# Optimization experiments

Hardware: AMD Instinct MI355X
Metric: run time of the kernel (lower is better)

## Reference

```python
import jax, jax.numpy as jnp
import numpy as np

N, E, G = 50000, 400000, 64   # nodes, edges, graphs
HEADS = 4
F_IN, H1, C3, OUT = 64, 96, 64, 10  # in feats, hidden (3*32), last conv out, classes


def seg_softmax(alpha, index, num_segments):
    # numerically stable softmax over segments (PyG softmax(alpha, edge_index_i))
    amax = jax.ops.segment_max(alpha, index, num_segments)
    amax = jnp.where(jnp.isfinite(amax), amax, 0.0)
    e = jnp.exp(alpha - amax[index])
    denom = jax.ops.segment_sum(e, index, num_segments)
    return e / (denom[index] + 1e-16)


def general_conv(x, src, dst, Wm, bm, att, Ws=None, bs=None):
    # GeneralConv (attention=True, additive, directed_msg, aggr='add')
    C = att.shape[-1]
    m = (x[src] @ Wm + bm).reshape(-1, HEADS, C)              # [E,H,C] gathered messages
    a = jax.nn.leaky_relu((m * att).sum(-1), 0.2)             # [E,H] attention logits
    a = seg_softmax(a, dst, N)                                # segment softmax per dest node
    agg = jax.ops.segment_sum(m * a[..., None], dst, N)       # [N,H,C] scatter-add
    out = agg.mean(axis=1)                                    # head mean -> [N,C]
    if Ws is None:                                            # lin_self = Identity (in==out)
        return out + x
    return out + x @ Ws + bs


def setup_inputs():
    key = jax.random.key(0)
    ks = jax.random.split(key, 16)
    s = 0.05
    return {
        "x": jax.random.normal(ks[0], (N, F_IN), jnp.float32),
        "edge_index": jax.random.randint(ks[1], (2, E), 0, N, jnp.int32),
        "batch": jnp.sort(jax.random.randint(ks[2], (N,), 0, G, jnp.int32)),
        # layer 1: F_IN -> H1
        "Wm1": jax.random.normal(ks[3], (F_IN, HEADS * H1), jnp.float32) * s,
        "bm1": jnp.zeros((HEADS * H1,), jnp.float32),
        "att1": jax.random.normal(ks[4], (HEADS, H1), jnp.float32) * s,
        "Ws1": jax.random.normal(ks[5], (F_IN, H1), jnp.float32) * s,
        "bs1": jnp.zeros((H1,), jnp.float32),
        # layer 2: H1 -> H1 (lin_self = Identity)
        "Wm2": jax.random.normal(ks[6], (H1, HEADS * H1), jnp.float32) * s,
        "bm2": jnp.zeros((HEADS * H1,), jnp.float32),
        "att2": jax.random.normal(ks[7], (HEADS, H1), jnp.float32) * s,
        # layer 3: H1 -> C3
        "Wm3": jax.random.normal(ks[8], (H1, HEADS * C3), jnp.float32) * s,
        "bm3": jnp.zeros((HEADS * C3,), jnp.float32),
        "att3": jax.random.normal(ks[9], (HEADS, C3), jnp.float32) * s,
        "Ws3": jax.random.normal(ks[10], (H1, C3), jnp.float32) * s,
        "bs3": jnp.zeros((C3,), jnp.float32),
        # classifier
        "Wfc": jax.random.normal(ks[11], (C3, OUT), jnp.float32) * s,
        "bfc": jnp.zeros((OUT,), jnp.float32),
    }


def reference(x, edge_index, batch, Wm1, bm1, att1, Ws1, bs1,
              Wm2, bm2, att2, Wm3, bm3, att3, Ws3, bs3, Wfc, bfc):
    src, dst = edge_index[0], edge_index[1]
    h = general_conv(x, src, dst, Wm1, bm1, att1, Ws1, bs1)
    h = general_conv(h, src, dst, Wm2, bm2, att2)
    h = general_conv(h, src, dst, Wm3, bm3, att3, Ws3, bs3)
    # global_mean_pool
    ssum = jax.ops.segment_sum(h, batch, G)
    cnt = jax.ops.segment_sum(jnp.ones((N, 1), h.dtype), batch, G)
    pooled = ssum / jnp.maximum(cnt, 1.0)                      # [G,C3]
    logits = pooled @ Wfc + bfc
    return jax.nn.log_softmax(logits, axis=1)
```

## Files before the change

kernel.cpp:

```cpp
#include <hip/hip_runtime.h>
#include <hip/hip_bf16.h>
#include <stdint.h>

using bf16 = __hip_bfloat16;
typedef __attribute__((ext_vector_type(8))) short bf16x8;
typedef __attribute__((ext_vector_type(4))) float f32x4;
typedef __attribute__((ext_vector_type(2))) float f32x2;

#define NN 50000
#define NE 400000
#define NG 64
#define FIN 64
#define HID 96
#define CC3 64
#define NOUT 10

#define SCAN_BLOCK 256
#define NPART ((NN + SCAN_BLOCK - 1) / SCAN_BLOCK)

__device__ __forceinline__ float b2f(bf16 h){ return __bfloat162float(h); }
__device__ __forceinline__ bf16 f2b(float f){ return __float2bfloat16(f); }
__device__ __forceinline__ float blo(unsigned v){ return __uint_as_float(v << 16); }
__device__ __forceinline__ float bhi(unsigned v){ return __uint_as_float(v & 0xFFFF0000u); }

struct PrepA {
  const float *Wm1,*att1,*bm1,*Wm2,*att2,*bm2,*Wm3,*att3,*bm3,*bs1;
  float *f2,*f3,*lbv,*zb; bf16* WTf1;
  int* deg; float* psum; int* done;
};
__global__ __launch_bounds__(256) void prep_a_kernel(PrepA j){
  int bid = blockIdx.x;
  if (bid == 0){
    for (int i=threadIdx.x; i<96*4; i+=256){
      int k=i>>2, h=i&3; float a=0.f;
      for (int c=0;c<96;++c) a += j.Wm2[k*384 + h*96 + c]*j.att2[h*96+c];
      j.f2[i]=a;
    }
    for (int i=threadIdx.x; i<96*4; i+=256){
      int k=i>>2, h=i&3; float a=0.f;
      for (int c=0;c<64;++c) a += j.Wm3[k*256 + h*64 + c]*j.att3[h*64+c];
      j.f3[i]=a;
    }
    for (int i=threadIdx.x; i<16*64; i+=256){
      int col=i>>6, k=i&63; float a=0.f;
      if (col<4){ for (int c=0;c<96;++c) a += j.Wm1[k*384 + col*96 + c]*j.att1[col*96+c]; }
      j.WTf1[i] = f2b(a);
    }
    if (threadIdx.x < 96) j.zb[threadIdx.x] = 0.f;
    __syncthreads();
    if (threadIdx.x < 4){
      int h = threadIdx.x;
      float l1=0.f,l2=0.f,l3=0.f;
      for (int c=0;c<96;++c) l1 += j.bm1[h*96+c]*j.att1[h*96+c];
      for (int c=0;c<96;++c) l2 += j.bm2[h*96+c]*j.att2[h*96+c];
      for (int c=0;c<64;++c) l3 += j.bm3[h*64+c]*j.att3[h*64+c];
      float e2 = l2;
      for (int k=0;k<96;++k) e2 += j.bs1[k]*j.f2[k*4+h];
      j.lbv[h]=l1; j.lbv[4+h]=e2; j.lbv[8+h]=l3;
    }
  } else if (bid <= NPART){
    int i=(bid-1)*256+threadIdx.x;
    if (i<NN) j.deg[i]=0;
  } else {
    for (int i=threadIdx.x; i<NG*CC3; i+=256) j.psum[i]=0.f;
    if (threadIdx.x==0) *j.done = 0;
  }
}

struct PrepB {
  const float *Wm1,*bm1,*Ws1,*Wm2,*bm2,*Wm3,*bm3,*Ws3;
  const float *f2,*f3;
  bf16 *WT1,*WT2,*WT3;
};
__device__ __forceinline__ float w1full(const PrepB& j, int k, int c){
  if (k < 256) return 0.25f*j.Wm1[(k&63)*384 + (k>>6)*96 + c];
  if (k == 256) return 0.25f*(j.bm1[c]+j.bm1[96+c]+j.bm1[192+c]+j.bm1[288+c]);
  if (k < 288) return 0.f;
  return j.Ws1[(k-288)*96 + c];
}
__device__ __forceinline__ float w2full(const PrepB& j, int k, int c){
  if (k < 384){ int kk=k%96, h=k/96; return 0.25f*j.Wm2[kk*384 + h*96 + c]; }
  if (k == 384) return 0.25f*(j.bm2[c]+j.bm2[96+c]+j.bm2[192+c]+j.bm2[288+c]);
  if (k < 416) return 0.f;
  return (k-416==c) ? 1.f : 0.f;
}
__device__ __forceinline__ float w3full(const PrepB& j, int k, int c){
  if (k < 384){ int kk=k%96, h=k/96; return 0.25f*j.Wm3[kk*256 + h*64 + c]; }
  if (k == 384) return 0.25f*(j.bm3[c]+j.bm3[64+c]+j.bm3[128+c]+j.bm3[192+c]);
  if (k < 416) return 0.f;
  return j.Ws3[(k-416)*64 + c];
}
__global__ __launch_bounds__(256) void prep_b_kernel(PrepB j){
  int idx = blockIdx.x*256 + threadIdx.x;
  if (idx < 112*384){
    int col = idx/384, k = idx - col*384;
    float v;
    if (k >= 352) v = 0.f;
    else if (col < 96) v = w1full(j,k,col);
    else if (col < 100){ int h=col-96; float a=0.f;
      for (int c=0;c<96;++c) a += w1full(j,k,c)*j.f2[c*4+h]; v=a; }
    else v = 0.f;
    j.WT1[col*384 + k] = f2b(v);
  } else if (idx < 112*384 + 112*512){
    int r = idx - 112*384;
    int col = r/512, k = r - col*512;
    float v;
    if (col < 96) v = w2full(j,k,col);
    else if (col < 100){ int h=col-96; float a=0.f;
      for (int c=0;c<96;++c) a += w2full(j,k,c)*j.f3[c*4+h]; v=a; }
    else v = 0.f;
    j.WT2[col*512 + k] = f2b(v);
  } else {
    int r = idx - 112*384 - 112*512;
    int col = r/512, k = r - col*512;
    j.WT3[col*512 + k] = f2b(w3full(j,k,col));
  }
}

__global__ void deg_kernel(const int* __restrict__ ei, int* __restrict__ deg){
  int e = blockIdx.x*256 + threadIdx.x;
  if (e < NE) atomicAdd(&deg[ei[NE + e]], 1);
}

__global__ __launch_bounds__(256) void scan_part_kernel(const int* __restrict__ deg,
    int* __restrict__ partials, int* __restrict__ done, int* __restrict__ off){
  __shared__ int ws[4];
  __shared__ int lastflag;
  __shared__ int buf[256];
  int i = blockIdx.x*SCAN_BLOCK + threadIdx.x;
  int v = (i < NN) ? deg[i] : 0;
  int lane = threadIdx.x & 63, w = threadIdx.x >> 6;
  int s = v;
  #pragma unroll
  for (int m=1;m<64;m<<=1) s += __shfl_xor(s,m);
  if (lane==0) ws[w]=s;
  __syncthreads();
  if (threadIdx.x==0){
    int tot = ws[0]+ws[1]+ws[2]+ws[3];
    atomicExch(&partials[blockIdx.x], tot);
    __threadfence();
    int old = atomicAdd(done, 1);
    lastflag = (old == NPART-1) ? 1 : 0;
  }
  __syncthreads();
  if (lastflag){
    int t = threadIdx.x;
    int pv = (t < NPART) ? atomicAdd(&partials[t], 0) : 0;
    buf[t] = pv; __syncthreads();
    for (int st=1; st<256; st<<=1){
      int x = (t>=st) ? buf[t-st] : 0;
      __syncthreads();
      buf[t] += x;
      __syncthreads();
    }
    if (t < NPART) atomicExch(&partials[t], buf[t] - pv);
    if (t == 0) off[NN] = buf[255];
  }
}

__global__ __launch_bounds__(256) void scan_final_kernel(const int* __restrict__ deg,
    const int* __restrict__ partials, int* __restrict__ off, int* __restrict__ cursor){
  __shared__ int buf[256];
  int i = blockIdx.x*SCAN_BLOCK + threadIdx.x;
  int t = threadIdx.x;
  int v = (i<NN) ? deg[i] : 0;
  buf[t] = v; __syncthreads();
  for (int s=1;s<256;s<<=1){
    int x = (t>=s) ? buf[t-s] : 0;
    __syncthreads();
    buf[t] += x;
    __syncthreads();
  }
  int ex = partials[blockIdx.x] + buf[t] - v;
  if (i<NN){ off[i]=ex; cursor[i]=ex; }
}

__global__ void scatter_kernel(const int* __restrict__ ei, int* __restrict__ cursor,
                               int* __restrict__ csr_src){
  int e = blockIdx.x*256 + threadIdx.x;
  if (e < NE){
    int d = ei[NE + e];
    int slot = atomicAdd(&cursor[d], 1);
    csr_src[slot] = ei[e];
  }
}

__global__ __launch_bounds__(256) void el1_kernel(const float* __restrict__ x,
    const bf16* __restrict__ WTf1, const float* __restrict__ lbv,
    bf16* __restrict__ xb, uint8_t* __restrict__ x8, float* __restrict__ EL)
{
  const int wave = threadIdx.x>>6, lane = threadIdx.x&63;
  const int tile = blockIdx.x*4 + wave;
  if (tile >= NN/16) return;
  const int lm = lane&15, q = lane>>4;
  const size_t row = (size_t)tile*16 + lm;
  bf16x8 xf[2];
  #pragma unroll
  for (int kt=0;kt<2;++kt){
    float4 a0 = *(const float4*)(x + row*64 + kt*32 + q*8);
    float4 a1 = *(const float4*)(x + row*64 + kt*32 + q*8 + 4);
    bf16 t[8] = {f2b(a0.x),f2b(a0.y),f2b(a0.z),f2b(a0.w),
                 f2b(a1.x),f2b(a1.y),f2b(a1.z),f2b(a1.w)};
    xf[kt] = *(const bf16x8*)t;
    *(bf16x8*)(xb + row*64 + kt*32 + q*8) = xf[kt];
    int p0 = 0, p1 = 0;
    p0 = __builtin_amdgcn_cvt_pk_fp8_f32(a0.x, a0.y, p0, false);
    p0 = __builtin_amdgcn_cvt_pk_fp8_f32(a0.z, a0.w, p0, true);
    p1 = __builtin_amdgcn_cvt_pk_fp8_f32(a1.x, a1.y, p1, false);
    p1 = __builtin_amdgcn_cvt_pk_fp8_f32(a1.z, a1.w, p1, true);
    uint2 pk; pk.x = (unsigned)p0; pk.y = (unsigned)p1;
    *(uint2*)(x8 + row*64 + kt*32 + q*8) = pk;
  }
  f32x4 acc = {};
  #pragma unroll
  for (int kt=0;kt<2;++kt){
    bf16x8 wf = *(const bf16x8*)(WTf1 + (size_t)lm*64 + kt*32 + q*8);
    acc = __builtin_amdgcn_mfma_f32_16x16x32_bf16(wf, xf[kt], acc, 0,0,0);
  }
  if (q==0){
    float4 e; float l;
    l=acc[0]+lbv[0]; l=(l>=0.f)?l:0.2f*l; e.x=__expf(fminf(fmaxf(l,-60.f),60.f));
    l=acc[1]+lbv[1]; l=(l>=0.f)?l:0.2f*l; e.y=__expf(fminf(fmaxf(l,-60.f),60.f));
    l=acc[2]+lbv[2]; l=(l>=0.f)?l:0.2f*l; e.z=__expf(fminf(fmaxf(l,-60.f),60.f));
    l=acc[3]+lbv[3]; l=(l>=0.f)?l:0.2f*l; e.w=__expf(fminf(fmaxf(l,-60.f),60.f));
    *(float4*)(EL + 4*row) = e;
  }
}

template<int KH>
__global__ __launch_bounds__(256) void agg_kernel(
    const int* __restrict__ off, const int* __restrict__ csr_src,
    const float* __restrict__ ELin, const uint8_t* __restrict__ T8,
    bf16* __restrict__ Sb)
{
  constexpr int R  = 4*KH;
  constexpr int KS = R + 32;
  const int wave = threadIdx.x >> 6, lane = threadIdx.x & 63;
  const int n = blockIdx.x*4 + wave;
  const int e0 = off[n], e1 = off[n+1];

  if (KH == 64){
    const int hidx = lane >> 4;
    const int kk = (4*lane) & 63;
    float acc[4] = {0.f,0.f,0.f,0.f};
    float dnl = 0.f;
    int base = e0;
    int cnt  = min(8, e1-base);
    int sreg = (base < e1 && lane < cnt) ? csr_src[base+lane] : 0;
    while (base < e1){
      const int nbase = base + 8;
      const int ncnt  = min(8, e1-nbase);
      int nreg = (nbase < e1 && lane < ncnt) ? csr_src[nbase+lane] : 0;
      int sv[8];
      #pragma unroll
      for (int j=0;j<8;++j) sv[j] = __shfl(sreg, j);
      float wl[8]; unsigned u[8];
      #pragma unroll
      for (int j=0;j<8;++j){
        wl[j] = ELin[4*(size_t)sv[j] + hidx];
        u[j]  = *(const unsigned*)(T8 + (size_t)sv[j]*64 + kk);
      }
      #pragma unroll
      for (int j=0;j<8;++j){
        float w = (j < cnt) ? wl[j] : 0.f;
        dnl += w;
        f32x2 a0 = __builtin_amdgcn_cvt_pk_f32_fp8((int)u[j], false);
        f32x2 a1 = __builtin_amdgcn_cvt_pk_f32_fp8((int)u[j], true);
        acc[0] += a0.x*w;  acc[1] += a0.y*w;
        acc[2] += a1.x*w;  acc[3] += a1.y*w;
      }
      sreg = nreg; cnt = ncnt; base = nbase;
    }
    const float rd = 1.f/(dnl + 1e-16f);
    bf16* srow = Sb + (size_t)n*KS;
    bf16 st[4] = {f2b(acc[0]*rd), f2b(acc[1]*rd), f2b(acc[2]*rd), f2b(acc[3]*rd)};
    *(uint2*)(srow + hidx*64 + kk) = *(const uint2*)st;
    if (lane < 8){
      uint2 z; z.x = 0u; z.y = 0u;
      if (lane == 0 && e1 > e0) z.x = 0x3F80u;
      *(uint2*)(srow + R + lane*4) = z;
    }
  } else {
    const bool act = (8*lane) < R;
    const int hidx = min(3, (8*lane)/KH);
    const int kk = (8*lane) % KH;
    float acc[8] = {0.f,0.f,0.f,0.f,0.f,0.f,0.f,0.f};
    float dnl = 0.f;
    int base = e0;
    int cnt  = min(8, e1-base);
    int sreg = (base < e1 && lane < cnt) ? csr_src[base+lane] : 0;
    while (base < e1){
      const int nbase = base + 8;
      const int ncnt  = min(8, e1-nbase);
      int nreg = (nbase < e1 && lane < ncnt) ? csr_src[nbase+lane] : 0;
      int sv[8];
      #pragma unroll
      for (int j=0;j<8;++j) sv[j] = __shfl(sreg, j);
      float wl[8]; uint2 u[8];
      #pragma unroll
      for (int j=0;j<8;++j){
        wl[j] = ELin[4*(size_t)sv[j] + hidx];
        u[j]  = *(const uint2*)(T8 + (size_t)sv[j]*KH + kk);
      }
      #pragma unroll
      for (int j=0;j<8;++j){
        float w = (j < cnt) ? wl[j] : 0.f;
        dnl += w;
        f32x2 a0 = __builtin_amdgcn_cvt_pk_f32_fp8((int)u[j].x, false);
        f32x2 a1 = __builtin_amdgcn_cvt_pk_f32_fp8((int)u[j].x, true);
        f32x2 a2 = __builtin_amdgcn_cvt_pk_f32_fp8((int)u[j].y, false);
        f32x2 a3 = __builtin_amdgcn_cvt_pk_f32_fp8((int)u[j].y, true);
        acc[0] += a0.x*w;  acc[1] += a0.y*w;
        acc[2] += a1.x*w;  acc[3] += a1.y*w;
        acc[4] += a2.x*w;  acc[5] += a2.y*w;
        acc[6] += a3.x*w;  acc[7] += a3.y*w;
      }
      sreg = nreg; cnt = ncnt; base = nbase;
    }
    const float rd = 1.f/(dnl + 1e-16f);
    bf16* srow = Sb + (size_t)n*KS;
    if (act){
      bf16 st[8];
      #pragma unroll
      for (int t=0;t<8;++t) st[t] = f2b(acc[t]*rd);
      *(bf16x8*)(srow + 8*lane) = *(const bf16x8*)st;
    } else if (8*lane < KS){
      bf16 st[8] = {};
      if (8*lane == R) st[0] = f2b((e1 > e0) ? 1.f : 0.f);
      *(bf16x8*)(srow + 8*lane) = *(const bf16x8*)st;
    }
  }
}

template<int KH, int NCT, bool POOL>
__global__ __launch_bounds__(256, 4) void gemm_kernel(
    const bf16* __restrict__ Sb, const bf16* __restrict__ Hprev,
    const bf16* __restrict__ WT, const float* __restrict__ bias,
    const float* __restrict__ lbe, bf16* __restrict__ Hout,
    uint8_t* __restrict__ H8out, float* __restrict__ ELout,
    const int* __restrict__ batch, float* __restrict__ psum)
{
  constexpr int R      = 4*KH;
  constexpr int KS     = R + 32;
  constexpr int KA     = KS + KH;
  constexpr int KTS    = KS/32;
  constexpr int NKT    = KA/32;
  constexpr int NCHUNK = (NKT + 3)/4;
  constexpr int KAP    = NCHUNK*128;
  constexpr int NCOL   = NCT*16;
  constexpr int NT     = NN/16;
  constexpr int WSZ    = NCOL*256;
  constexpr int OSZ    = POOL ? (4*16*68*4) : (4*16*104*2);
  constexpr int USZ    = (WSZ > OSZ) ? WSZ : OSZ;
  __shared__ __align__(16) unsigned char lds[USZ];

  const int tid  = threadIdx.x;
  const int wave = tid >> 6, lane = tid & 63;
  const int lm = lane & 15, q = lane >> 4;
  const int tile = blockIdx.x*4 + wave;
  const bool active = (tile < NT);
  const size_t row = (size_t)tile*16 + lm;

  const bf16* arow = Sb + row*KS;
  const bf16* hrow = Hprev + row*KH;
  const unsigned sw = (unsigned)((lm & 7) << 4);

  f32x4 acc[NCT];
  #pragma unroll
  for (int c=0;c<NCT;++c) acc[c] = (f32x4){0.f,0.f,0.f,0.f};

  #pragma unroll
  for (int chunk=0; chunk<NCHUNK; ++chunk){
    if (chunk) __syncthreads();
    {
      const int k0 = chunk*128;
      for (int idx = tid; idx < NCOL*16; idx += 256){
        const int col = idx >> 4, sg = idx & 15;
        uint4 v = *(const uint4*)(WT + (size_t)col*KAP + k0 + sg*8);
        const unsigned off = (unsigned)(sg*16) ^ (unsigned)((col & 7) << 4);
        *(uint4*)(lds + col*256 + off) = v;
      }
    }
    __syncthreads();
    if (active){
      bf16x8 a[4];
      #pragma unroll
      for (int t=0;t<4;++t){
        const int kt = chunk*4 + t;
        if (kt < KTS)      a[t] = *(const bf16x8*)(arow + kt*32 + q*8);
        else if (kt < NKT) a[t] = *(const bf16x8*)(hrow + (kt-KTS)*32 + q*8);
        else { bf16 z[8] = {}; a[t] = *(const bf16x8*)z; }
      }
      #pragma unroll
      for (int ct=0; ct<NCT; ++ct){
        const unsigned char* rbase = lds + (ct*16 + lm)*256;
        #pragma unroll
        for (int t=0;t<4;++t){
          bf16x8 wf = *(const bf16x8*)(rbase + (((unsigned)(t*64 + q*16)) ^ sw));
          acc[ct] = __builtin_amdgcn_mfma_f32_16x16x32_bf16(wf, a[t], acc[ct], 0,0,0);
        }
      }
    }
  }
  __syncthreads();

  if (active){
    if (!POOL){
      unsigned short* ob = (unsigned short*)(lds) + wave*16*104;
      #pragma unroll
      for (int ct=0; ct<NCT-1; ++ct){
        const int c = ct*16 + q*4;
        bf16 st[4] = {f2b(acc[ct][0]+bias[c]),   f2b(acc[ct][1]+bias[c+1]),
                      f2b(acc[ct][2]+bias[c+2]), f2b(acc[ct][3]+bias[c+3])};
        *(uint2*)(ob + lm*104 + c) = *(const uint2*)st;
      }
      if (q == 0){
        float4 e; float l;
        l=acc[NCT-1][0]+lbe[0]; l=(l>=0.f)?l:0.2f*l; e.x=__expf(fminf(fmaxf(l,-60.f),60.f));
        l=acc[NCT-1][1]+lbe[1]; l=(l>=0.f)?l:0.2f*l; e.y=__expf(fminf(fmaxf(l,-60.f),60.f));
        l=acc[NCT-1][2]+lbe[2]; l=(l>=0.f)?l:0.2f*l; e.z=__expf(fminf(fmaxf(l,-60.f),60.f));
        l=acc[NCT-1][3]+lbe[3]; l=(l>=0.f)?l:0.2f*l; e.w=__expf(fminf(fmaxf(l,-60.f),60.f));
        *(float4*)(ELout + 4*row) = e;
      }
      __builtin_amdgcn_wave_barrier();
      const size_t n0w = (size_t)tile*16;
      #pragma unroll
      for (int jj=0; jj<3; ++jj){
        const int idx = jj*64 + lane;
        const int r = idx/12, ch = idx - r*12;
        uint4 v = *(const uint4*)(ob + r*104 + ch*8);
        *(uint4*)(Hout + (n0w+r)*96 + ch*8) = v;
        int p0 = 0, p1 = 0;
        p0 = __builtin_amdgcn_cvt_pk_fp8_f32(blo(v.x), bhi(v.x), p0, false);
        p0 = __builtin_amdgcn_cvt_pk_fp8_f32(blo(v.y), bhi(v.y), p0, true);
        p1 = __builtin_amdgcn_cvt_pk_fp8_f32(blo(v.z), bhi(v.z), p1, false);
        p1 = __builtin_amdgcn_cvt_pk_fp8_f32(blo(v.w), bhi(v.w), p1, true);
        uint2 pk; pk.x = (unsigned)p0; pk.y = (unsigned)p1;
        *(uint2*)(H8out + (n0w+r)*96 + ch*8) = pk;
      }
    } else {
      float* ob = (float*)(lds) + wave*16*68;
      #pragma unroll
      for (int ct=0; ct<NCT; ++ct){
        const int c = ct*16 + q*4;
        float* orow = ob + lm*68;
        orow[c]   = acc[ct][0]+bias[c];   orow[c+1] = acc[ct][1]+bias[c+1];
        orow[c+2] = acc[ct][2]+bias[c+2]; orow[c+3] = acc[ct][3]+bias[c+3];
      }
      int bload = (lane < 16) ? batch[tile*16 + lane] : 0;
      __builtin_amdgcn_wave_barrier();
      const int c = lane;
      int curg = __shfl(bload, 0); float a = 0.f;
      #pragma unroll
      for (int i=0;i<16;++i){
        float v = ob[i*68 + c];
        int g = __shfl(bload, i);
        if (g != curg){ atomicAdd(&psum[curg*64+c], a); a=0.f; curg=g; }
        a += v;
      }
      atomicAdd(&psum[curg*64+c], a);
    }
  }
}

__global__ __launch_bounds__(64) void fc_kernel(const float* __restrict__ psum,
    const int* __restrict__ batch, const float* __restrict__ Wfc,
    const float* __restrict__ bfc, float* __restrict__ out){
  int g = blockIdx.x, t = threadIdx.x;
  __shared__ int sb[2];
  if (t < 2){
    int target = g + t;
    int lo=0, hi=NN;
    while (lo<hi){ int mid=(lo+hi)>>1; if (batch[mid]<target) lo=mid+1; else hi=mid; }
    sb[t]=lo;
  }
  __syncthreads();
  float cnt = (float)(sb[1]-sb[0]);
  __shared__ float p[CC3];
  __shared__ float lg[NOUT];
  p[t] = psum[g*CC3 + t] / fmaxf(cnt, 1.0f);
  __syncthreads();
  if (t < NOUT){
    float a = bfc[t];
    for (int c=0;c<CC3;++c) a += p[c]*Wfc[c*NOUT + t];
    lg[t] = a;
  }
  __syncthreads();
  if (t < NOUT){
    float m = -INFINITY;
    #pragma unroll
    for (int i=0;i<NOUT;++i) m = fmaxf(m, lg[i]);
    float s = 0.f;
    #pragma unroll
    for (int i=0;i<NOUT;++i) s += __expf(lg[i]-m);
    out[g*NOUT + t] = lg[t] - m - __logf(s);
  }
}

extern "C" void kernel_launch(void* const* d_in, const int* in_sizes, int n_in,
                              void* d_out, int out_size, void* d_ws, size_t ws_size,
                              hipStream_t stream) {
  const float* xf    = (const float*)d_in[0];
  const int*   ei    = (const int*)d_in[1];
  const int*   batch = (const int*)d_in[2];
  const float* pWm1  = (const float*)d_in[3];
  const float* pbm1  = (const float*)d_in[4];
  const float* patt1 = (const float*)d_in[5];
  const float* pWs1  = (const float*)d_in[6];
  const float* pbs1  = (const float*)d_in[7];
  const float* pWm2  = (const float*)d_in[8];
  const float* pbm2  = (const float*)d_in[9];
  const float* patt2 = (const float*)d_in[10];
  const float* pWm3  = (const float*)d_in[11];
  const float* pbm3  = (const float*)d_in[12];
  const float* patt3 = (const float*)d_in[13];
  const float* pWs3  = (const float*)d_in[14];
  const float* pbs3  = (const float*)d_in[15];
  const float* pWfc  = (const float*)d_in[16];
  const float* pbfc  = (const float*)d_in[17];

  char* p = (char*)d_ws;
  auto alloc = [&](size_t bytes)->char*{ char* q = p; p += (bytes + 255) & ~(size_t)255; return q; };
  int*     deg     = (int*)  alloc(NN*sizeof(int));
  int*     off     = (int*)  alloc((NN+1)*sizeof(int));
  int*     cursor  = (int*)  alloc(NN*sizeof(int));
  int*     csr_src = (int*)  alloc(NE*sizeof(int));
  int*     partials= (int*)  alloc(NPART*sizeof(int));
  int*     done    = (int*)  alloc(sizeof(int));
  float*   ELa     = (float*)alloc((size_t)NN*4*sizeof(float));
  float*   ELb     = (float*)alloc((size_t)NN*4*sizeof(float));
  bf16*    xb      = (bf16*) alloc((size_t)NN*64*sizeof(bf16));
  uint8_t* x8      = (uint8_t*)alloc((size_t)NN*64);
  uint8_t* H8      = (uint8_t*)alloc((size_t)NN*96);
  bf16*    H1b     = (bf16*) alloc((size_t)NN*96*sizeof(bf16));
  bf16*    H2b     = (bf16*) alloc((size_t)NN*96*sizeof(bf16));
  bf16*    Sb      = (bf16*) alloc((size_t)NN*416*sizeof(bf16));
  float*   psum    = (float*)alloc((size_t)NG*CC3*sizeof(float));
  float*   f2      = (float*)alloc(96*4*sizeof(float));
  float*   f3      = (float*)alloc(96*4*sizeof(float));
  float*   lbv     = (float*)alloc(12*sizeof(float));
  float*   zb      = (float*)alloc(96*sizeof(float));
  bf16*    WTf1    = (bf16*) alloc((size_t)16*64*sizeof(bf16));
  bf16*    WT1     = (bf16*) alloc((size_t)112*384*sizeof(bf16));
  bf16*    WT2     = (bf16*) alloc((size_t)112*512*sizeof(bf16));
  bf16*    WT3     = (bf16*) alloc((size_t)64*512*sizeof(bf16));

  PrepA pa;
  pa.Wm1=pWm1; pa.att1=patt1; pa.bm1=pbm1;
  pa.Wm2=pWm2; pa.att2=patt2; pa.bm2=pbm2;
  pa.Wm3=pWm3; pa.att3=patt3; pa.bm3=pbm3;
  pa.bs1=pbs1; pa.f2=f2; pa.f3=f3; pa.lbv=lbv; pa.zb=zb; pa.WTf1=WTf1;
  pa.deg=deg; pa.psum=psum; pa.done=done;
  prep_a_kernel<<<NPART+2, 256, 0, stream>>>(pa);

  PrepB pb;
  pb.Wm1=pWm1; pb.bm1=pbm1; pb.Ws1=pWs1;
  pb.Wm2=pWm2; pb.bm2=pbm2;
  pb.Wm3=pWm3; pb.bm3=pbm3; pb.Ws3=pWs3;
  pb.f2=f2; pb.f3=f3; pb.WT1=WT1; pb.WT2=WT2; pb.WT3=WT3;
  prep_b_kernel<<<(112*384 + 112*512 + 64*512)/256, 256, 0, stream>>>(pb);

  deg_kernel<<<(NE+255)/256, 256, 0, stream>>>(ei, deg);
  scan_part_kernel<<<NPART, 256, 0, stream>>>(deg, partials, done, off);
  scan_final_kernel<<<NPART, 256, 0, stream>>>(deg, partials, off, cursor);
  scatter_kernel<<<(NE+255)/256, 256, 0, stream>>>(ei, cursor, csr_src);

  el1_kernel<<<(NN/16+3)/4, 256, 0, stream>>>(xf, WTf1, lbv, xb, x8, ELa);

  const int AGB = NN/4;
  const int GGB = (NN/16 + 3)/4;

  agg_kernel<64><<<AGB, 256, 0, stream>>>(off, csr_src, ELa, x8, Sb);
  gemm_kernel<64,7,false><<<GGB, 256, 0, stream>>>(Sb, xb, WT1, pbs1, lbv+4,
                                                   H1b, H8, ELb, batch, psum);
  agg_kernel<96><<<AGB, 256, 0, stream>>>(off, csr_src, ELb, H8, Sb);
  gemm_kernel<96,7,false><<<GGB, 256, 0, stream>>>(Sb, H1b, WT2, zb, lbv+8,
                                                   H2b, H8, ELa, batch, psum);
  agg_kernel<96><<<AGB, 256, 0, stream>>>(off, csr_src, ELa, H8, Sb);
  gemm_kernel<96,4,true ><<<GGB, 256, 0, stream>>>(Sb, H2b, WT3, pbs3, nullptr,
                                                   nullptr, nullptr, nullptr, batch, psum);

  fc_kernel<<<NG, 64, 0, stream>>>(psum, batch, pWfc, pbfc, (float*)d_out);
}
```

Measured before the change: 337.1 us.

## Fuse el1 into prep_b launch and hoist gemm A-operand loads out of chunk loop

```diff
diff --git a/kernel.cpp b/kernel.cpp
--- a/kernel.cpp
+++ b/kernel.cpp
@@ -17,6 +17,8 @@
 
 #define SCAN_BLOCK 256
 #define NPART ((NN + SCAN_BLOCK - 1) / SCAN_BLOCK)
+#define PBW ((112*384 + 112*512 + 64*512)/256)
+#define ELB ((NN/16 + 3)/4)
 
 __device__ __forceinline__ float b2f(bf16 h){ return __bfloat162float(h); }
 __device__ __forceinline__ bf16 f2b(float f){ return __float2bfloat16(f); }
@@ -71,6 +73,8 @@
   const float *Wm1,*bm1,*Ws1,*Wm2,*bm2,*Wm3,*bm3,*Ws3;
   const float *f2,*f3;
   bf16 *WT1,*WT2,*WT3;
+  const float* x; const bf16* WTf1; const float* lbv;
+  bf16* xb; uint8_t* x8; float* EL;
 };
 __device__ __forceinline__ float w1full(const PrepB& j, int k, int c){
   if (k < 256) return 0.25f*j.Wm1[(k&63)*384 + (k>>6)*96 + c];
@@ -91,29 +95,69 @@
   return j.Ws3[(k-416)*64 + c];
 }
 __global__ __launch_bounds__(256) void prep_b_kernel(PrepB j){
-  int idx = blockIdx.x*256 + threadIdx.x;
-  if (idx < 112*384){
-    int col = idx/384, k = idx - col*384;
-    float v;
-    if (k >= 352) v = 0.f;
-    else if (col < 96) v = w1full(j,k,col);
-    else if (col < 100){ int h=col-96; float a=0.f;
-      for (int c=0;c<96;++c) a += w1full(j,k,c)*j.f2[c*4+h]; v=a; }
-    else v = 0.f;
-    j.WT1[col*384 + k] = f2b(v);
-  } else if (idx < 112*384 + 112*512){
-    int r = idx - 112*384;
-    int col = r/512, k = r - col*512;
-    float v;
-    if (col < 96) v = w2full(j,k,col);
-    else if (col < 100){ int h=col-96; float a=0.f;
-      for (int c=0;c<96;++c) a += w2full(j,k,c)*j.f3[c*4+h]; v=a; }
-    else v = 0.f;
-    j.WT2[col*512 + k] = f2b(v);
+  const int bid = blockIdx.x;
+  if (bid < PBW){
+    int idx = bid*256 + threadIdx.x;
+    if (idx < 112*384){
+      int col = idx/384, k = idx - col*384;
+      float v;
+      if (k >= 352) v = 0.f;
+      else if (col < 96) v = w1full(j,k,col);
+      else if (col < 100){ int h=col-96; float a=0.f;
+        for (int c=0;c<96;++c) a += w1full(j,k,c)*j.f2[c*4+h]; v=a; }
+      else v = 0.f;
+      j.WT1[col*384 + k] = f2b(v);
+    } else if (idx < 112*384 + 112*512){
+      int r = idx - 112*384;
+      int col = r/512, k = r - col*512;
+      float v;
+      if (col < 96) v = w2full(j,k,col);
+      else if (col < 100){ int h=col-96; float a=0.f;
+        for (int c=0;c<96;++c) a += w2full(j,k,c)*j.f3[c*4+h]; v=a; }
+      else v = 0.f;
+      j.WT2[col*512 + k] = f2b(v);
+    } else {
+      int r = idx - 112*384 - 112*512;
+      int col = r/512, k = r - col*512;
+      j.WT3[col*512 + k] = f2b(w3full(j,k,col));
+    }
   } else {
-    int r = idx - 112*384 - 112*512;
-    int col = r/512, k = r - col*512;
-    j.WT3[col*512 + k] = f2b(w3full(j,k,col));
+    const int wave = threadIdx.x>>6, lane = threadIdx.x&63;
+    const int tile = (bid - PBW)*4 + wave;
+    if (tile >= NN/16) return;
+    const int lm = lane&15, q = lane>>4;
+    const size_t row = (size_t)tile*16 + lm;
+    bf16x8 xf[2];
+    #pragma unroll
+    for (int kt=0;kt<2;++kt){
+      float4 a0 = *(const float4*)(j.x + row*64 + kt*32 + q*8);
+      float4 a1 = *(const float4*)(j.x + row*64 + kt*32 + q*8 + 4);
+      bf16 t[8] = {f2b(a0.x),f2b(a0.y),f2b(a0.z),f2b(a0.w),
+                   f2b(a1.x),f2b(a1.y),f2b(a1.z),f2b(a1.w)};
+      xf[kt] = *(const bf16x8*)t;
+      *(bf16x8*)(j.xb + row*64 + kt*32 + q*8) = xf[kt];
+      int p0 = 0, p1 = 0;
+      p0 = __builtin_amdgcn_cvt_pk_fp8_f32(a0.x, a0.y, p0, false);
+      p0 = __builtin_amdgcn_cvt_pk_fp8_f32(a0.z, a0.w, p0, true);
+      p1 = __builtin_amdgcn_cvt_pk_fp8_f32(a1.x, a1.y, p1, false);
+      p1 = __builtin_amdgcn_cvt_pk_fp8_f32(a1.z, a1.w, p1, true);
+      uint2 pk; pk.x = (unsigned)p0; pk.y = (unsigned)p1;
+      *(uint2*)(j.x8 + row*64 + kt*32 + q*8) = pk;
+    }
+    f32x4 acc = {};
+    #pragma unroll
+    for (int kt=0;kt<2;++kt){
+      bf16x8 wf = *(const bf16x8*)(j.WTf1 + (size_t)lm*64 + kt*32 + q*8);
+      acc = __builtin_amdgcn_mfma_f32_16x16x32_bf16(wf, xf[kt], acc, 0,0,0);
+    }
+    if (q==0){
+      float4 e; float l;
+      l=acc[0]+j.lbv[0]; l=(l>=0.f)?l:0.2f*l; e.x=__expf(fminf(fmaxf(l,-60.f),60.f));
+      l=acc[1]+j.lbv[1]; l=(l>=0.f)?l:0.2f*l; e.y=__expf(fminf(fmaxf(l,-60.f),60.f));
+      l=acc[2]+j.lbv[2]; l=(l>=0.f)?l:0.2f*l; e.z=__expf(fminf(fmaxf(l,-60.f),60.f));
+      l=acc[3]+j.lbv[3]; l=(l>=0.f)?l:0.2f*l; e.w=__expf(fminf(fmaxf(l,-60.f),60.f));
+      *(float4*)(j.EL + 4*row) = e;
+    }
   }
 }
 
@@ -185,48 +229,6 @@
   }
 }
 
-__global__ __launch_bounds__(256) void el1_kernel(const float* __restrict__ x,
-    const bf16* __restrict__ WTf1, const float* __restrict__ lbv,
-    bf16* __restrict__ xb, uint8_t* __restrict__ x8, float* __restrict__ EL)
-{
-  const int wave = threadIdx.x>>6, lane = threadIdx.x&63;
-  const int tile = blockIdx.x*4 + wave;
-  if (tile >= NN/16) return;
-  const int lm = lane&15, q = lane>>4;
-  const size_t row = (size_t)tile*16 + lm;
-  bf16x8 xf[2];
-  #pragma unroll
-  for (int kt=0;kt<2;++kt){
-    float4 a0 = *(const float4*)(x + row*64 + kt*32 + q*8);
-    float4 a1 = *(const float4*)(x + row*64 + kt*32 + q*8 + 4);
-    bf16 t[8] = {f2b(a0.x),f2b(a0.y),f2b(a0.z),f2b(a0.w),
-                 f2b(a1.x),f2b(a1.y),f2b(a1.z),f2b(a1.w)};
-    xf[kt] = *(const bf16x8*)t;
-    *(bf16x8*)(xb + row*64 + kt*32 + q*8) = xf[kt];
-    int p0 = 0, p1 = 0;
-    p0 = __builtin_amdgcn_cvt_pk_fp8_f32(a0.x, a0.y, p0, false);
-    p0 = __builtin_amdgcn_cvt_pk_fp8_f32(a0.z, a0.w, p0, true);
-    p1 = __builtin_amdgcn_cvt_pk_fp8_f32(a1.x, a1.y, p1, false);
-    p1 = __builtin_amdgcn_cvt_pk_fp8_f32(a1.z, a1.w, p1, true);
-    uint2 pk; pk.x = (unsigned)p0; pk.y = (unsigned)p1;
-    *(uint2*)(x8 + row*64 + kt*32 + q*8) = pk;
-  }
-  f32x4 acc = {};
-  #pragma unroll
-  for (int kt=0;kt<2;++kt){
-    bf16x8 wf = *(const bf16x8*)(WTf1 + (size_t)lm*64 + kt*32 + q*8);
-    acc = __builtin_amdgcn_mfma_f32_16x16x32_bf16(wf, xf[kt], acc, 0,0,0);
-  }
-  if (q==0){
-    float4 e; float l;
-    l=acc[0]+lbv[0]; l=(l>=0.f)?l:0.2f*l; e.x=__expf(fminf(fmaxf(l,-60.f),60.f));
-    l=acc[1]+lbv[1]; l=(l>=0.f)?l:0.2f*l; e.y=__expf(fminf(fmaxf(l,-60.f),60.f));
-    l=acc[2]+lbv[2]; l=(l>=0.f)?l:0.2f*l; e.z=__expf(fminf(fmaxf(l,-60.f),60.f));
-    l=acc[3]+lbv[3]; l=(l>=0.f)?l:0.2f*l; e.w=__expf(fminf(fmaxf(l,-60.f),60.f));
-    *(float4*)(EL + 4*row) = e;
-  }
-}
-
 template<int KH>
 __global__ __launch_bounds__(256) void agg_kernel(
     const int* __restrict__ off, const int* __restrict__ csr_src,
@@ -333,7 +335,7 @@
 }
 
 template<int KH, int NCT, bool POOL>
-__global__ __launch_bounds__(256, 4) void gemm_kernel(
+__global__ __launch_bounds__(256, 3) void gemm_kernel(
     const bf16* __restrict__ Sb, const bf16* __restrict__ Hprev,
     const bf16* __restrict__ WT, const float* __restrict__ bias,
     const float* __restrict__ lbe, bf16* __restrict__ Hout,
@@ -359,11 +361,18 @@
   const int lm = lane & 15, q = lane >> 4;
   const int tile = blockIdx.x*4 + wave;
   const bool active = (tile < NT);
-  const size_t row = (size_t)tile*16 + lm;
+  const int ctile = active ? tile : (NT-1);
+  const size_t row = (size_t)ctile*16 + lm;
 
   const bf16* arow = Sb + row*KS;
   const bf16* hrow = Hprev + row*KH;
   const unsigned sw = (unsigned)((lm & 7) << 4);
+
+  bf16x8 a[NKT];
+  #pragma unroll
+  for (int kt=0; kt<KTS; ++kt) a[kt] = *(const bf16x8*)(arow + kt*32 + q*8);
+  #pragma unroll
+  for (int kt=KTS; kt<NKT; ++kt) a[kt] = *(const bf16x8*)(hrow + (kt-KTS)*32 + q*8);
 
   f32x4 acc[NCT];
   #pragma unroll
@@ -374,7 +383,9 @@
     if (chunk) __syncthreads();
     {
       const int k0 = chunk*128;
-      for (int idx = tid; idx < NCOL*16; idx += 256){
+      #pragma unroll
+      for (int it=0; it<NCOL*16/256; ++it){
+        const int idx = it*256 + tid;
         const int col = idx >> 4, sg = idx & 15;
         uint4 v = *(const uint4*)(WT + (size_t)col*KAP + k0 + sg*8);
         const unsigned off = (unsigned)(sg*16) ^ (unsigned)((col & 7) << 4);
@@ -382,22 +393,15 @@
       }
     }
     __syncthreads();
-    if (active){
-      bf16x8 a[4];
+    #pragma unroll
+    for (int ct=0; ct<NCT; ++ct){
+      const unsigned char* rbase = lds + (ct*16 + lm)*256;
       #pragma unroll
       for (int t=0;t<4;++t){
         const int kt = chunk*4 + t;
-        if (kt < KTS)      a[t] = *(const bf16x8*)(arow + kt*32 + q*8);
-        else if (kt < NKT) a[t] = *(const bf16x8*)(hrow + (kt-KTS)*32 + q*8);
-        else { bf16 z[8] = {}; a[t] = *(const bf16x8*)z; }
-      }
-      #pragma unroll
-      for (int ct=0; ct<NCT; ++ct){
-        const unsigned char* rbase = lds + (ct*16 + lm)*256;
-        #pragma unroll
-        for (int t=0;t<4;++t){
+        if (kt < NKT){
           bf16x8 wf = *(const bf16x8*)(rbase + (((unsigned)(t*64 + q*16)) ^ sw));
-          acc[ct] = __builtin_amdgcn_mfma_f32_16x16x32_bf16(wf, a[t], acc[ct], 0,0,0);
+          acc[ct] = __builtin_amdgcn_mfma_f32_16x16x32_bf16(wf, a[kt], acc[ct], 0,0,0);
         }
       }
     }
@@ -450,15 +454,15 @@
       int bload = (lane < 16) ? batch[tile*16 + lane] : 0;
       __builtin_amdgcn_wave_barrier();
       const int c = lane;
-      int curg = __shfl(bload, 0); float a = 0.f;
+      int curg = __shfl(bload, 0); float a2 = 0.f;
       #pragma unroll
       for (int i=0;i<16;++i){
         float v = ob[i*68 + c];
         int g = __shfl(bload, i);
-        if (g != curg){ atomicAdd(&psum[curg*64+c], a); a=0.f; curg=g; }
-        a += v;
-      }
-      atomicAdd(&psum[curg*64+c], a);
+        if (g != curg){ atomicAdd(&psum[curg*64+c], a2); a2=0.f; curg=g; }
+        a2 += v;
+      }
+      atomicAdd(&psum[curg*64+c], a2);
     }
   }
 }
@@ -558,14 +562,13 @@
   pb.Wm2=pWm2; pb.bm2=pbm2;
   pb.Wm3=pWm3; pb.bm3=pbm3; pb.Ws3=pWs3;
   pb.f2=f2; pb.f3=f3; pb.WT1=WT1; pb.WT2=WT2; pb.WT3=WT3;
-  prep_b_kernel<<<(112*384 + 112*512 + 64*512)/256, 256, 0, stream>>>(pb);
+  pb.x=xf; pb.WTf1=WTf1; pb.lbv=lbv; pb.xb=xb; pb.x8=x8; pb.EL=ELa;
+  prep_b_kernel<<<PBW + ELB, 256, 0, stream>>>(pb);
 
   deg_kernel<<<(NE+255)/256, 256, 0, stream>>>(ei, deg);
   scan_part_kernel<<<NPART, 256, 0, stream>>>(deg, partials, done, off);
   scan_final_kernel<<<NPART, 256, 0, stream>>>(deg, partials, off, cursor);
   scatter_kernel<<<(NE+255)/256, 256, 0, stream>>>(ei, cursor, csr_src);
-
-  el1_kernel<<<(NN/16+3)/4, 256, 0, stream>>>(xf, WTf1, lbv, xb, x8, ELa);
 
   const int AGB = NN/4;
   const int GGB = (NN/16 + 3)/4;
```

After: 326.6 us. 1.03x faster.
